# Optimization experiments

Measured on AMD Instinct MI355X. Metric: run time of the kernel, lower is better.

Reference implementation:

```python
import jax, jax.numpy as jnp
import numpy as np

EPS = 1e-12  # torch F.normalize eps


def rms_norm(x, g):
    # x: (b, c, l); normalize over channel dim, scale by g * sqrt(c)
    c = x.shape[1]
    n = jnp.sqrt(jnp.sum(x * x, axis=1, keepdims=True))
    return x / jnp.maximum(n, EPS) * g * jnp.sqrt(jnp.asarray(c, x.dtype))


def setup_inputs() -> dict:
    key = jax.random.key(0)
    ks = jax.random.split(key, 4)
    b, c, l = 4, 256, 2048
    heads, dim_head = 8, 64
    hidden = heads * dim_head
    x = jax.random.normal(ks[0], (b, c, l), dtype=jnp.float32)
    g1 = jnp.ones((1, c, 1), dtype=jnp.float32)
    w_qkv = jax.random.normal(ks[1], (hidden * 3, c), dtype=jnp.float32) * (c ** -0.5)
    w_out = jax.random.normal(ks[2], (c, hidden), dtype=jnp.float32) * (hidden ** -0.5)
    b_out = jnp.zeros((c,), dtype=jnp.float32)
    g2 = jnp.ones((1, c, 1), dtype=jnp.float32)
    return {"x": x, "g1": g1, "w_qkv": w_qkv, "w_out": w_out, "b_out": b_out, "g2": g2}


def reference(x, g1, w_qkv, w_out, b_out, g2):
    heads, dim_head = 8, 64
    scale = dim_head ** -0.5
    b, c, l = x.shape

    xn = rms_norm(x, g1)
    qkv = jnp.einsum('oc,bcl->bol', w_qkv, xn)  # (b, 3*hidden, l)
    q, k, v = jnp.split(qkv, 3, axis=1)
    # (b, h*d, l) -> (b, h, d, l)
    q = q.reshape(b, heads, dim_head, l) * scale
    k = k.reshape(b, heads, dim_head, l)
    v = v.reshape(b, heads, dim_head, l)

    sim = jnp.einsum('bhci,bhcj->bhij', q, k)          # (b, h, l, l)
    attn = jax.nn.softmax(sim, axis=-1)                # stable softmax (max-subtract)
    y = jnp.einsum('bhij,bhdj->bhid', attn, v)         # (b, h, l, d)

    # rearrange 'b h l d -> b (h d) l'
    y = jnp.transpose(y, (0, 1, 3, 2)).reshape(b, heads * dim_head, l)
    out = jnp.einsum('oc,bcl->bol', w_out, y) + b_out[None, :, None]
    return rms_norm(out, g2)
```

## Files before the change

kernel.cpp:

```cpp
#include <hip/hip_runtime.h>
#include <cstdint>
#include <cstddef>

using s16x4  = __attribute__((ext_vector_type(4))) short;
using short8 = __attribute__((ext_vector_type(8))) short;
using f32x4  = __attribute__((ext_vector_type(4))) float;
using f32x16 = __attribute__((ext_vector_type(16))) float;
using u32x4  = __attribute__((ext_vector_type(4))) unsigned int;

#define DEV static __device__ __forceinline__

constexpr int Bn = 4, Cn = 256, Ln = 2048, Hn = 8, Dn = 64, HIDn = 512;

DEV unsigned short f2bf(float f){
  union { float f; uint32_t u; } v; v.f = f;
  uint32_t u = v.u;
  return (unsigned short)((u + 0x7FFFu + ((u >> 16) & 1u)) >> 16);
}

DEV uint32_t cvtpk(float lo, float hi){
  uint32_t r;
  asm("v_cvt_pk_bf16_f32 %0, %1, %2" : "=v"(r) : "v"(lo), "v"(hi));
  return r;
}

DEV void gl16(const unsigned short* g, unsigned short* l){
  __builtin_amdgcn_global_load_lds((const __attribute__((address_space(1))) void*)g,
                                   (__attribute__((address_space(3))) void*)l, 16, 0, 0);
}

template<int NCHUNK, int RS>
DEV void stage_panel(const unsigned short* gbase, unsigned short* lbase, int tid, int wv){
  #pragma unroll
  for (int i = 0; i < NCHUNK; i += 256){
    int chunk = i + tid;
    int row = chunk >> 3, c = chunk & 7;
    gl16(gbase + (size_t)row * RS + ((c ^ (row & 7)) * 8),
         lbase + (i + wv * 64) * 8);
  }
}

DEV short8 fragr(const char* base, int row, int ch){
  return *reinterpret_cast<const short8*>(base + row * 128 + ((ch ^ (row & 7)) << 4));
}

__global__ __launch_bounds__(256) void k_xt2(const float* __restrict__ x,
                                             const float* __restrict__ g1,
                                             unsigned short* __restrict__ xT,
                                             const float* __restrict__ wqkv,
                                             unsigned short* __restrict__ wqkv_b,
                                             const float* __restrict__ wout,
                                             unsigned short* __restrict__ wout_b){
  int bid = blockIdx.x;
  int tid = threadIdx.x;
  if (bid >= 128){
    if (bid < 512){
      int idx = (bid - 128) * 256 + tid;
      #pragma unroll
      for (int it = 0; it < 4; ++it){ wqkv_b[idx] = f2bf(wqkv[idx]); idx += 98304; }
    } else {
      int idx = (bid - 512) * 256 + tid;
      #pragma unroll
      for (int it = 0; it < 4; ++it){ wout_b[idx] = f2bf(wout[idx]); idx += 32768; }
    }
    return;
  }
  __shared__ float xs[4][64][65];
  __shared__ float ps[4][64];
  __shared__ float sl[64];
  int b  = bid >> 5;
  int l0 = (bid & 31) * 64;
  int i = tid >> 6, j = tid & 63;
  #pragma unroll
  for (int ct = 0; ct < 4; ++ct){
    const float* xp = x + ((size_t)(b * Cn + ct * 64) * Ln) + l0;
    #pragma unroll
    for (int it = 0; it < 16; ++it){
      int row = i + it * 4;
      xs[ct][row][j] = xp[(size_t)row * Ln + j];
    }
  }
  __syncthreads();
  {
    int lp = tid & 63, cq = tid >> 6;
    float a = 0.f;
    #pragma unroll 8
    for (int cc = 0; cc < 64; ++cc){ float v = xs[cq][cc][lp]; a += v * v; }
    ps[cq][lp] = a;
  }
  __syncthreads();
  if (tid < 64){
    float t = ps[0][tid] + ps[1][tid] + ps[2][tid] + ps[3][tid];
    sl[tid] = 16.0f / fmaxf(sqrtf(t), 1e-12f);
  }
  __syncthreads();
  int jj = tid >> 2, part = tid & 3;
  float sc = sl[jj];
  #pragma unroll
  for (int ct = 0; ct < 4; ++ct){
    unsigned short* op = xT + ((size_t)(b * Ln + l0 + jj)) * Cn + ct * 64 + part * 16;
    #pragma unroll
    for (int hb = 0; hb < 2; ++hb){
      short8 pack;
      #pragma unroll
      for (int m = 0; m < 8; ++m){
        int c = part * 16 + hb * 8 + m;
        pack[m] = (short)f2bf(xs[ct][c][jj] * sc * g1[ct * 64 + c]);
      }
      *reinterpret_cast<short8*>(op + hb * 8) = pack;
    }
  }
}

__global__ __launch_bounds__(256) void k_gemm_qkv(const unsigned short* __restrict__ xT,
                                                  const unsigned short* __restrict__ w,
                                                  unsigned short* __restrict__ qb,
                                                  unsigned short* __restrict__ kb,
                                                  unsigned short* __restrict__ vb){
  __shared__ alignas(16) char smem[49152];
  int b  = blockIdx.z;
  int l0 = blockIdx.x * 128;
  int tid = threadIdx.x;
  int wv = tid >> 6, lane = tid & 63;
  int grp = lane >> 4, lc = lane & 15;
  const unsigned short* xb = xT + (size_t)b * Ln * Cn;

  if (blockIdx.y < 16){
    int n0 = blockIdx.y * 64;
    int lwl = (wv >> 1) * 64, nwl = (wv & 1) * 32;
    unsigned short* As = (unsigned short*)smem;
    unsigned short* Bs = (unsigned short*)(smem + 32768);
    f32x4 acc[4][2] = {};
    stage_panel<1024, Cn>(xb + (size_t)l0 * Cn, As, tid, wv);
    stage_panel<512,  Cn>(w  + (size_t)n0 * Cn, Bs, tid, wv);
    asm volatile("s_waitcnt vmcnt(0)" ::: "memory");
    __syncthreads();
    #pragma unroll
    for (int s = 0; s < 4; ++s){
      if (s < 3){
        stage_panel<1024, Cn>(xb + (size_t)l0 * Cn + (s + 1) * 64, As + ((s + 1) & 1) * 8192, tid, wv);
        stage_panel<512,  Cn>(w  + (size_t)n0 * Cn + (s + 1) * 64, Bs + ((s + 1) & 1) * 4096, tid, wv);
      }
      const char* Ab = (const char*)(As + (s & 1) * 8192);
      const char* Bb = (const char*)(Bs + (s & 1) * 4096);
      #pragma unroll
      for (int kk = 0; kk < 2; ++kk){
        short8 afr[4], bfr[2];
        #pragma unroll
        for (int mt = 0; mt < 4; ++mt) afr[mt] = fragr(Ab, lwl + mt * 16 + lc, kk * 4 + grp);
        #pragma unroll
        for (int nt = 0; nt < 2; ++nt) bfr[nt] = fragr(Bb, nwl + nt * 16 + lc, kk * 4 + grp);
        #pragma unroll
        for (int mt = 0; mt < 4; ++mt)
          #pragma unroll
          for (int nt = 0; nt < 2; ++nt)
            acc[mt][nt] = __builtin_amdgcn_mfma_f32_16x16x32_bf16(afr[mt], bfr[nt], acc[mt][nt], 0, 0, 0);
      }
      asm volatile("s_waitcnt vmcnt(0)" ::: "memory");
      __syncthreads();
    }
    const float QSCALE = 0.125f * 1.4426950408889634f;
    #pragma unroll
    for (int mt = 0; mt < 4; ++mt)
      #pragma unroll
      for (int nt = 0; nt < 2; ++nt)
        #pragma unroll
        for (int r = 0; r < 4; ++r){
          int l = l0 + lwl + mt * 16 + grp * 4 + r;
          int o = n0 + nwl + nt * 16 + lc;
          float v = acc[mt][nt][r];
          if (o < HIDn){
            size_t idx = (((size_t)(b * Hn + (o >> 6)) * Ln + l) << 6) | (size_t)(o & 63);
            qb[idx] = f2bf(v * QSCALE);
          } else {
            int o2 = o - HIDn;
            size_t idx = (((size_t)(b * Hn + (o2 >> 6)) * Ln + l) << 6) | (size_t)(o2 & 63);
            kb[idx] = f2bf(v);
          }
        }
  } else {
    int m0 = (blockIdx.y - 16) * 64;
    int mwl = (wv >> 1) * 32, lwl = (wv & 1) * 64;
    const unsigned short* wvp = w + (size_t)1024 * Cn;
    unsigned short* Av = (unsigned short*)smem;
    unsigned short* Bv = (unsigned short*)(smem + 16384);
    f32x4 acc[2][4] = {};
    stage_panel<512,  Cn>(wvp + (size_t)m0 * Cn, Av, tid, wv);
    stage_panel<1024, Cn>(xb  + (size_t)l0 * Cn, Bv, tid, wv);
    asm volatile("s_waitcnt vmcnt(0)" ::: "memory");
    __syncthreads();
    #pragma unroll
    for (int s = 0; s < 4; ++s){
      if (s < 3){
        stage_panel<512,  Cn>(wvp + (size_t)m0 * Cn + (s + 1) * 64, Av + ((s + 1) & 1) * 4096, tid, wv);
        stage_panel<1024, Cn>(xb  + (size_t)l0 * Cn + (s + 1) * 64, Bv + ((s + 1) & 1) * 8192, tid, wv);
      }
      const char* Ab = (const char*)(Av + (s & 1) * 4096);
      const char* Bb = (const char*)(Bv + (s & 1) * 8192);
      #pragma unroll
      for (int kk = 0; kk < 2; ++kk){
        short8 afr[2], bfr[4];
        #pragma unroll
        for (int mt = 0; mt < 2; ++mt) afr[mt] = fragr(Ab, mwl + mt * 16 + lc, kk * 4 + grp);
        #pragma unroll
        for (int nt = 0; nt < 4; ++nt) bfr[nt] = fragr(Bb, lwl + nt * 16 + lc, kk * 4 + grp);
        #pragma unroll
        for (int mt = 0; mt < 2; ++mt)
          #pragma unroll
          for (int nt = 0; nt < 4; ++nt)
            acc[mt][nt] = __builtin_amdgcn_mfma_f32_16x16x32_bf16(afr[mt], bfr[nt], acc[mt][nt], 0, 0, 0);
      }
      asm volatile("s_waitcnt vmcnt(0)" ::: "memory");
      __syncthreads();
    }
    #pragma unroll
    for (int mt = 0; mt < 2; ++mt)
      #pragma unroll
      for (int nt = 0; nt < 4; ++nt)
        #pragma unroll
        for (int r = 0; r < 4; ++r){
          int o = m0 + mwl + mt * 16 + grp * 4 + r;
          int l = l0 + lwl + nt * 16 + lc;
          vb[((size_t)(b * HIDn + o)) * Ln + l] = f2bf(acc[mt][nt][r]);
        }
  }
}

__global__ __launch_bounds__(256, 2) void k_attn(const unsigned short* __restrict__ qb,
                                                 const unsigned short* __restrict__ kb,
                                                 const unsigned short* __restrict__ vb,
                                                 unsigned short* __restrict__ yb){
  int wid = (blockIdx.x & 7) * 64 + (blockIdx.x >> 3);
  int qt = wid & 15;
  int bh = wid >> 4;
  int b = bh >> 3, h = bh & 7;
  int tid = threadIdx.x;
  int wv = tid >> 6, lane = tid & 63;
  int ln = lane & 31, hi = lane >> 5;

  const unsigned short* qp = qb + (size_t)bh * Ln * Dn;
  const unsigned short* kp = kb + (size_t)bh * Ln * Dn;
  const unsigned short* vp = vb + ((size_t)(b * HIDn + h * Dn)) * Ln;
  unsigned short* yp = yb + (size_t)b * Ln * HIDn + h * Dn;

  __shared__ alignas(16) unsigned short KR[3][4096];
  __shared__ alignas(16) unsigned short VR[5][4096];

  int lrow = lane >> 3, lcol = lane & 7;
  int chunk = lcol ^ lrow;
  int srow = wv * 16 + lrow;
  const unsigned short* kg = kp + (size_t)srow * Dn + chunk * 8;
  const unsigned short* vg = vp + (size_t)srow * Ln + chunk * 8;
  int ldK = wv * 1024;

  int q = qt * 128 + wv * 32 + ln;
  int sw = (ln & 7) << 4;

  f32x16 accO[2] = {};
  f32x16 sA[2], sB[2];
  u32x4 Wsv[4];
  float lsv[16] = {};
  const f32x16 ZV = {};

  auto DMA = [&](int tile, int kslot, int vslot){
    const unsigned short* kgn = kg + (size_t)tile * 64 * Dn;
    const unsigned short* vgn = vg + (size_t)tile * 64;
    unsigned short* Kd = &KR[kslot][ldK];
    unsigned short* Vd = &VR[vslot][ldK];
    gl16(kgn,          Kd);
    gl16(kgn + 8 * Dn, Kd + 512);
    gl16(vgn,          Vd);
    gl16(vgn + 8 * Ln, Vd + 512);
  };

  DMA(0, 0, 0);
  DMA(1, 1, 1);
  DMA(2, 2, 2);
  short8 qf[4];
  #pragma unroll
  for (int s = 0; s < 4; ++s)
    qf[s] = *reinterpret_cast<const short8*>(qp + (size_t)q * Dn + s * 16 + hi * 8);
  asm volatile("s_waitcnt vmcnt(0)" ::: "memory");
  __builtin_amdgcn_s_barrier();

  auto QK = [&](int kslot, f32x16 (&sN)[2]){
    const char* Kc = (const char*)&KR[kslot][0];
    sN[0] = ZV; sN[1] = ZV;
    __builtin_amdgcn_s_setprio(1);
    #pragma unroll
    for (int kb2 = 0; kb2 < 2; ++kb2){
      const char* Kr = Kc + (kb2 * 32 + ln) * 128;
      #pragma unroll
      for (int s = 0; s < 4; ++s){
        short8 kf = *reinterpret_cast<const short8*>(Kr + ((s * 32 + hi * 16) ^ sw));
        sN[kb2] = __builtin_amdgcn_mfma_f32_32x32x16_bf16(kf, qf[s], sN[kb2], 0, 0, 0);
      }
    }
    __builtin_amdgcn_s_setprio(0);
  };

  auto PV = [&](int vslot){
    const char* Vc = (const char*)&VR[vslot][0];
    __builtin_amdgcn_s_setprio(1);
    #pragma unroll
    for (int c = 0; c < 4; ++c){
      short8 Bf = __builtin_bit_cast(short8, Wsv[c]);
      #pragma unroll
      for (int db = 0; db < 2; ++db){
        const char* Vr = Vc + (db * 32 + ln) * 128;
        s16x4 a0 = *reinterpret_cast<const s16x4*>(Vr + ((c * 32) ^ sw) + hi * 8);
        s16x4 a1 = *reinterpret_cast<const s16x4*>(Vr + ((c * 32 + 16) ^ sw) + hi * 8);
        short8 Af = {a0[0], a0[1], a0[2], a0[3], a1[0], a1[1], a1[2], a1[3]};
        accO[db] = __builtin_amdgcn_mfma_f32_32x32x16_bf16(Af, Bf, accO[db], 0, 0, 0);
      }
    }
    __builtin_amdgcn_s_setprio(0);
  };

  auto SM = [&](f32x16 (&sC)[2]){
    #pragma unroll
    for (int r = 0; r < 16; ++r){
      float p0, p1;
      asm("v_exp_f32 %0, %1" : "=v"(p0) : "v"(sC[0][r]));
      asm("v_exp_f32 %0, %1" : "=v"(p1) : "v"(sC[1][r]));
      sC[0][r] = p0; sC[1][r] = p1;
      lsv[r] += p0 + p1;
    }
    #pragma unroll
    for (int c = 0; c < 4; ++c){
      int base = (c & 1) * 8, kb2 = c >> 1;
      Wsv[c][0] = cvtpk(sC[kb2][base + 0], sC[kb2][base + 1]);
      Wsv[c][1] = cvtpk(sC[kb2][base + 2], sC[kb2][base + 3]);
      Wsv[c][2] = cvtpk(sC[kb2][base + 4], sC[kb2][base + 5]);
      Wsv[c][3] = cvtpk(sC[kb2][base + 6], sC[kb2][base + 7]);
    }
  };

  QK(0, sA);

  auto ITER = [&](int t, f32x16 (&sC)[2], f32x16 (&sN)[2]){
    int tl = t + 3 > 31 ? 31 : t + 3;
    DMA(tl, (t + 3) % 3, (t + 3) % 5);
    if (t + 1 < 32) QK((t + 1) % 3, sN);
    if (t > 0)      PV((t - 1) % 5);
    SM(sC);
    asm volatile("s_waitcnt vmcnt(4)" ::: "memory");
    __builtin_amdgcn_s_barrier();
  };

  for (int t = 0; t < 32; t += 2){
    ITER(t,     sA, sB);
    ITER(t + 1, sB, sA);
  }
  PV(31 % 5);

  #pragma unroll
  for (int st = 8; st >= 1; st >>= 1)
    #pragma unroll
    for (int r = 0; r < st; ++r) lsv[r] += lsv[r + st];
  float lsum = lsv[0] + __shfl_xor(lsv[0], 32, 64);
  float inv = 1.0f / lsum;
  #pragma unroll
  for (int db = 0; db < 2; ++db)
    #pragma unroll
    for (int rq = 0; rq < 4; ++rq){
      uint32_t w0 = cvtpk(accO[db][rq * 4 + 0] * inv, accO[db][rq * 4 + 1] * inv);
      uint32_t w1 = cvtpk(accO[db][rq * 4 + 2] * inv, accO[db][rq * 4 + 3] * inv);
      int dd = db * 32 + rq * 8 + hi * 4;
      uint32_t* dst = reinterpret_cast<uint32_t*>(yp + (size_t)q * HIDn + dd);
      dst[0] = w0; dst[1] = w1;
    }
}

__global__ __launch_bounds__(256) void k_out(const unsigned short* __restrict__ yb,
                                             const unsigned short* __restrict__ w,
                                             const float* __restrict__ bias,
                                             const float* __restrict__ g2,
                                             float* __restrict__ out){
  __shared__ alignas(16) unsigned short Ws[2][16384];
  __shared__ float cs[4][16];
  __shared__ float sc2[16];
  int b  = blockIdx.y;
  int l0 = blockIdx.x * 16;
  int tid = threadIdx.x;
  int wv = tid >> 6, lane = tid & 63;
  int grp = lane >> 4, lc = lane & 15;
  int mw = wv * 64;
  f32x4 acc[4] = {};
  const unsigned short* ybp = yb + (size_t)b * Ln * HIDn + (size_t)l0 * HIDn;

  stage_panel<2048, HIDn>(w, Ws[0], tid, wv);
  asm volatile("s_waitcnt vmcnt(0)" ::: "memory");
  __syncthreads();
  #pragma unroll
  for (int s = 0; s < 8; ++s){
    if (s < 7) stage_panel<2048, HIDn>(w + (s + 1) * 64, Ws[(s + 1) & 1], tid, wv);
    const char* Ab = (const char*)Ws[s & 1];
    #pragma unroll
    for (int kk = 0; kk < 2; ++kk){
      int kc = s * 64 + kk * 32 + grp * 8;
      short8 afr[4];
      #pragma unroll
      for (int mt = 0; mt < 4; ++mt) afr[mt] = fragr(Ab, mw + mt * 16 + lc, kk * 4 + grp);
      short8 bfr = *reinterpret_cast<const short8*>(ybp + (size_t)lc * HIDn + kc);
      #pragma unroll
      for (int mt = 0; mt < 4; ++mt)
        acc[mt] = __builtin_amdgcn_mfma_f32_16x16x32_bf16(afr[mt], bfr, acc[mt], 0, 0, 0);
    }
    asm volatile("s_waitcnt vmcnt(0)" ::: "memory");
    __syncthreads();
  }

  float part = 0.f;
  #pragma unroll
  for (int mt = 0; mt < 4; ++mt)
    #pragma unroll
    for (int r = 0; r < 4; ++r){
      int o = mw + mt * 16 + grp * 4 + r;
      float v = acc[mt][r] + bias[o];
      acc[mt][r] = v;
      part += v * v;
    }
  part += __shfl_xor(part, 16, 64);
  part += __shfl_xor(part, 32, 64);
  if (lane < 16) cs[wv][lc] = part;
  __syncthreads();
  if (tid < 16){
    float t = cs[0][tid] + cs[1][tid] + cs[2][tid] + cs[3][tid];
    sc2[tid] = 16.0f / fmaxf(sqrtf(t), 1e-12f);
  }
  __syncthreads();
  float s2 = sc2[lc];
  #pragma unroll
  for (int mt = 0; mt < 4; ++mt)
    #pragma unroll
    for (int r = 0; r < 4; ++r){
      int o = mw + mt * 16 + grp * 4 + r;
      int l = l0 + lc;
      out[((size_t)(b * Cn + o)) * Ln + l] = acc[mt][r] * s2 * g2[o];
    }
}

extern "C" void kernel_launch(void* const* d_in, const int* in_sizes, int n_in,
                              void* d_out, int out_size, void* d_ws, size_t ws_size,
                              hipStream_t stream){
  const float* x     = (const float*)d_in[0];
  const float* g1    = (const float*)d_in[1];
  const float* w_qkv = (const float*)d_in[2];
  const float* w_out = (const float*)d_in[3];
  const float* b_out = (const float*)d_in[4];
  const float* g2    = (const float*)d_in[5];

  char* wsb = (char*)d_ws;
  unsigned short* wqkv_b = (unsigned short*)(wsb + 0);
  unsigned short* wout_b = (unsigned short*)(wsb + 786432);
  unsigned short* xT     = (unsigned short*)(wsb + 1081344);
  unsigned short* qbuf   = (unsigned short*)(wsb + 5275648);
  unsigned short* kbuf   = (unsigned short*)(wsb + 13664256);
  unsigned short* vbuf   = (unsigned short*)(wsb + 22052864);
  unsigned short* ybuf   = (unsigned short*)(wsb + 30441472);

  k_xt2<<<640, 256, 0, stream>>>(x, g1, xT, w_qkv, wqkv_b, w_out, wout_b);
  k_gemm_qkv<<<dim3(16, 24, 4), 256, 0, stream>>>(xT, wqkv_b, qbuf, kbuf, vbuf);
  k_attn<<<512, 256, 0, stream>>>(qbuf, kbuf, vbuf, ybuf);
  k_out<<<dim3(128, 4), 256, 0, stream>>>(ybuf, wout_b, b_out, g2, (float*)d_out);
}
```

Before: 81.58 us.

## Split attention key range across two wave groups per block and merge partials

The attention kernel now launches 512 threads per block. Two groups of four waves each process half of the 2048 keys, using 32-key tiles in their own shared-memory ring buffers. At the end, the second half writes its partial output and row sums to shared memory, and the first half adds them, normalizes and stores. This doubles the waves per block to raise occupancy and latency hiding, at the cost of a shared-memory reduction, smaller MFMA work per tile and higher register pressure under the new launch bounds.

```diff
diff --git a/kernel.cpp b/kernel.cpp
--- a/kernel.cpp
+++ b/kernel.cpp
@@ -226,7 +226,7 @@
   }
 }
 
-__global__ __launch_bounds__(256, 2) void k_attn(const unsigned short* __restrict__ qb,
+__global__ __launch_bounds__(512, 4) void k_attn(const unsigned short* __restrict__ qb,
                                                  const unsigned short* __restrict__ kb,
                                                  const unsigned short* __restrict__ vb,
                                                  unsigned short* __restrict__ yb){
@@ -236,6 +236,7 @@
   int b = bh >> 3, h = bh & 7;
   int tid = threadIdx.x;
   int wv = tid >> 6, lane = tid & 63;
+  int half = wv >> 2, ws = wv & 3;
   int ln = lane & 31, hi = lane >> 5;
 
   const unsigned short* qp = qb + (size_t)bh * Ln * Dn;
@@ -243,39 +244,33 @@
   const unsigned short* vp = vb + ((size_t)(b * HIDn + h * Dn)) * Ln;
   unsigned short* yp = yb + (size_t)b * Ln * HIDn + h * Dn;
 
-  __shared__ alignas(16) unsigned short KR[3][4096];
-  __shared__ alignas(16) unsigned short VR[5][4096];
-
-  int lrow = lane >> 3, lcol = lane & 7;
-  int chunk = lcol ^ lrow;
-  int srow = wv * 16 + lrow;
-  const unsigned short* kg = kp + (size_t)srow * Dn + chunk * 8;
-  const unsigned short* vg = vp + (size_t)srow * Ln + chunk * 8;
-  int ldK = wv * 1024;
-
-  int q = qt * 128 + wv * 32 + ln;
-  int sw = (ln & 7) << 4;
+  __shared__ alignas(16) char SMEM[65536];
+
+  int krow = ws * 8 + (lane >> 3);
+  int kchunk = (lane & 7) ^ (krow & 7);
+  const unsigned short* kgl = kp + (size_t)(half * 1024 + krow) * Dn + kchunk * 8;
+  int vrow = ws * 16 + (lane >> 2);
+  int vchunk = (lane & 3) ^ (vrow & 3);
+  const unsigned short* vgl = vp + (size_t)vrow * Ln + half * 1024 + vchunk * 8;
+
+  int q = qt * 128 + ws * 32 + ln;
+  int swK = (ln & 7) << 4;
+  int swV = (ln & 3) << 4;
 
   f32x16 accO[2] = {};
-  f32x16 sA[2], sB[2];
-  u32x4 Wsv[4];
-  float lsv[16] = {};
+  f32x16 sA, sB;
+  u32x4 Wsv[2];
+  float lsv[4] = {};
   const f32x16 ZV = {};
 
-  auto DMA = [&](int tile, int kslot, int vslot){
-    const unsigned short* kgn = kg + (size_t)tile * 64 * Dn;
-    const unsigned short* vgn = vg + (size_t)tile * 64;
-    unsigned short* Kd = &KR[kslot][ldK];
-    unsigned short* Vd = &VR[vslot][ldK];
-    gl16(kgn,          Kd);
-    gl16(kgn + 8 * Dn, Kd + 512);
-    gl16(vgn,          Vd);
-    gl16(vgn + 8 * Ln, Vd + 512);
+  auto DMA = [&](int t){
+    unsigned short* Kd = (unsigned short*)(SMEM + (half * 3 + t % 3) * 4096 + ws * 1024);
+    unsigned short* Vd = (unsigned short*)(SMEM + 24576 + (half * 5 + t % 5) * 4096 + ws * 1024);
+    gl16(kgl + (size_t)t * 32 * Dn, Kd);
+    gl16(vgl + (size_t)t * 32, Vd);
   };
 
-  DMA(0, 0, 0);
-  DMA(1, 1, 1);
-  DMA(2, 2, 2);
+  DMA(0); DMA(1); DMA(2);
   short8 qf[4];
   #pragma unroll
   for (int s = 0; s < 4; ++s)
@@ -283,33 +278,29 @@
   asm volatile("s_waitcnt vmcnt(0)" ::: "memory");
   __builtin_amdgcn_s_barrier();
 
-  auto QK = [&](int kslot, f32x16 (&sN)[2]){
-    const char* Kc = (const char*)&KR[kslot][0];
-    sN[0] = ZV; sN[1] = ZV;
+  auto QK = [&](int t, f32x16& sN){
+    const char* Kr = SMEM + (half * 3 + t % 3) * 4096 + ln * 128;
+    sN = ZV;
     __builtin_amdgcn_s_setprio(1);
     #pragma unroll
-    for (int kb2 = 0; kb2 < 2; ++kb2){
-      const char* Kr = Kc + (kb2 * 32 + ln) * 128;
-      #pragma unroll
-      for (int s = 0; s < 4; ++s){
-        short8 kf = *reinterpret_cast<const short8*>(Kr + ((s * 32 + hi * 16) ^ sw));
-        sN[kb2] = __builtin_amdgcn_mfma_f32_32x32x16_bf16(kf, qf[s], sN[kb2], 0, 0, 0);
-      }
+    for (int s = 0; s < 4; ++s){
+      short8 kf = *reinterpret_cast<const short8*>(Kr + ((s * 32 + hi * 16) ^ swK));
+      sN = __builtin_amdgcn_mfma_f32_32x32x16_bf16(kf, qf[s], sN, 0, 0, 0);
     }
     __builtin_amdgcn_s_setprio(0);
   };
 
-  auto PV = [&](int vslot){
-    const char* Vc = (const char*)&VR[vslot][0];
+  auto PV = [&](int t){
+    const char* Vc = SMEM + 24576 + (half * 5 + t % 5) * 4096;
     __builtin_amdgcn_s_setprio(1);
     #pragma unroll
-    for (int c = 0; c < 4; ++c){
+    for (int c = 0; c < 2; ++c){
       short8 Bf = __builtin_bit_cast(short8, Wsv[c]);
       #pragma unroll
       for (int db = 0; db < 2; ++db){
-        const char* Vr = Vc + (db * 32 + ln) * 128;
-        s16x4 a0 = *reinterpret_cast<const s16x4*>(Vr + ((c * 32) ^ sw) + hi * 8);
-        s16x4 a1 = *reinterpret_cast<const s16x4*>(Vr + ((c * 32 + 16) ^ sw) + hi * 8);
+        const char* Vr = Vc + (db * 32 + ln) * 64;
+        s16x4 a0 = *reinterpret_cast<const s16x4*>(Vr + ((c * 32) ^ swV) + hi * 8);
+        s16x4 a1 = *reinterpret_cast<const s16x4*>(Vr + ((c * 32 + 16) ^ swV) + hi * 8);
         short8 Af = {a0[0], a0[1], a0[2], a0[3], a1[0], a1[1], a1[2], a1[3]};
         accO[db] = __builtin_amdgcn_mfma_f32_32x32x16_bf16(Af, Bf, accO[db], 0, 0, 0);
       }
@@ -317,34 +308,31 @@
     __builtin_amdgcn_s_setprio(0);
   };
 
-  auto SM = [&](f32x16 (&sC)[2]){
+  auto SM = [&](f32x16& sC){
     #pragma unroll
     for (int r = 0; r < 16; ++r){
-      float p0, p1;
-      asm("v_exp_f32 %0, %1" : "=v"(p0) : "v"(sC[0][r]));
-      asm("v_exp_f32 %0, %1" : "=v"(p1) : "v"(sC[1][r]));
-      sC[0][r] = p0; sC[1][r] = p1;
-      lsv[r] += p0 + p1;
-    }
-    #pragma unroll
-    for (int c = 0; c < 4; ++c){
-      int base = (c & 1) * 8, kb2 = c >> 1;
-      Wsv[c][0] = cvtpk(sC[kb2][base + 0], sC[kb2][base + 1]);
-      Wsv[c][1] = cvtpk(sC[kb2][base + 2], sC[kb2][base + 3]);
-      Wsv[c][2] = cvtpk(sC[kb2][base + 4], sC[kb2][base + 5]);
-      Wsv[c][3] = cvtpk(sC[kb2][base + 6], sC[kb2][base + 7]);
+      float p;
+      asm("v_exp_f32 %0, %1" : "=v"(p) : "v"(sC[r]));
+      sC[r] = p;
+      lsv[r & 3] += p;
+    }
+    #pragma unroll
+    for (int c = 0; c < 2; ++c){
+      Wsv[c][0] = cvtpk(sC[c * 8 + 0], sC[c * 8 + 1]);
+      Wsv[c][1] = cvtpk(sC[c * 8 + 2], sC[c * 8 + 3]);
+      Wsv[c][2] = cvtpk(sC[c * 8 + 4], sC[c * 8 + 5]);
+      Wsv[c][3] = cvtpk(sC[c * 8 + 6], sC[c * 8 + 7]);
     }
   };
 
   QK(0, sA);
 
-  auto ITER = [&](int t, f32x16 (&sC)[2], f32x16 (&sN)[2]){
-    int tl = t + 3 > 31 ? 31 : t + 3;
-    DMA(tl, (t + 3) % 3, (t + 3) % 5);
-    if (t + 1 < 32) QK((t + 1) % 3, sN);
-    if (t > 0)      PV((t - 1) % 5);
+  auto ITER = [&](int t, f32x16& sC, f32x16& sN){
+    if (t + 3 < 32) DMA(t + 3);
+    if (t + 1 < 32) QK(t + 1, sN);
+    if (t > 0)      PV(t - 1);
     SM(sC);
-    asm volatile("s_waitcnt vmcnt(4)" ::: "memory");
+    asm volatile("s_waitcnt vmcnt(2)" ::: "memory");
     __builtin_amdgcn_s_barrier();
   };
 
@@ -352,24 +340,39 @@
     ITER(t,     sA, sB);
     ITER(t + 1, sB, sA);
   }
-  PV(31 % 5);
-
-  #pragma unroll
-  for (int st = 8; st >= 1; st >>= 1)
-    #pragma unroll
-    for (int r = 0; r < st; ++r) lsv[r] += lsv[r + st];
-  float lsum = lsv[0] + __shfl_xor(lsv[0], 32, 64);
-  float inv = 1.0f / lsum;
-  #pragma unroll
-  for (int db = 0; db < 2; ++db)
-    #pragma unroll
-    for (int rq = 0; rq < 4; ++rq){
-      uint32_t w0 = cvtpk(accO[db][rq * 4 + 0] * inv, accO[db][rq * 4 + 1] * inv);
-      uint32_t w1 = cvtpk(accO[db][rq * 4 + 2] * inv, accO[db][rq * 4 + 3] * inv);
+  PV(31);
+
+  float lpart = (lsv[0] + lsv[1]) + (lsv[2] + lsv[3]);
+  float lsum = lpart + __shfl_xor(lpart, 32, 64);
+  float* mo = (float*)SMEM;
+  float* SL = (float*)(SMEM + 32768);
+  __syncthreads();
+  if (half == 1){
+    #pragma unroll
+    for (int r4 = 0; r4 < 8; ++r4){
+      int db = r4 >> 2, rq = r4 & 3;
+      f32x4 v = { accO[db][rq * 4 + 0], accO[db][rq * 4 + 1],
+                  accO[db][rq * 4 + 2], accO[db][rq * 4 + 3] };
+      *reinterpret_cast<f32x4*>(&mo[(ws * 8 + r4) * 256 + lane * 4]) = v;
+    }
+    if (hi == 0) SL[ws * 32 + ln] = lsum;
+  }
+  __syncthreads();
+  if (half == 0){
+    float inv = 1.0f / (lsum + SL[ws * 32 + ln]);
+    #pragma unroll
+    for (int r4 = 0; r4 < 8; ++r4){
+      int db = r4 >> 2, rq = r4 & 3;
+      f32x4 o1 = *reinterpret_cast<const f32x4*>(&mo[(ws * 8 + r4) * 256 + lane * 4]);
+      uint32_t w0 = cvtpk((accO[db][rq * 4 + 0] + o1[0]) * inv,
+                          (accO[db][rq * 4 + 1] + o1[1]) * inv);
+      uint32_t w1 = cvtpk((accO[db][rq * 4 + 2] + o1[2]) * inv,
+                          (accO[db][rq * 4 + 3] + o1[3]) * inv);
       int dd = db * 32 + rq * 8 + hi * 4;
       uint32_t* dst = reinterpret_cast<uint32_t*>(yp + (size_t)q * HIDn + dd);
       dst[0] = w0; dst[1] = w1;
     }
+  }
 }
 
 __global__ __launch_bounds__(256) void k_out(const unsigned short* __restrict__ yb,
@@ -462,6 +465,6 @@
 
   k_xt2<<<640, 256, 0, stream>>>(x, g1, xT, w_qkv, wqkv_b, w_out, wout_b);
   k_gemm_qkv<<<dim3(16, 24, 4), 256, 0, stream>>>(xT, wqkv_b, qbuf, kbuf, vbuf);
-  k_attn<<<512, 256, 0, stream>>>(qbuf, kbuf, vbuf, ybuf);
+  k_attn<<<512, 512, 0, stream>>>(qbuf, kbuf, vbuf, ybuf);
   k_out<<<dim3(128, 4), 256, 0, stream>>>(ybuf, wout_b, b_out, g2, (float*)d_out);
 }
```

New measurement: 95.39 us. 16.9% more time.
